# Kernel optimization log

Hardware: AMD Instinct MI355X
Metric: run time of the kernel (lower is better)

Reference implementation:

```python
import jax, jax.numpy as jnp
import numpy as np

E, C, FE, FS, K = 8, 1024, 1024, 4096, 2  # n_experts, embed, expert_inter, shared_inter, top_k
B, T = 4, 2048

def setup_inputs() -> dict:
    key = jax.random.key(0)
    ks = jax.random.split(key, 8)
    def init(k, shape, fan_in):
        return jax.random.normal(k, shape, jnp.float32) / np.sqrt(fan_in).astype(np.float32)
    return dict(
        x=jax.random.normal(ks[0], (B, T, C), jnp.float32),
        gate_w=init(ks[1], (E, C), C),        # nn.Linear(C, E, bias=False).weight
        ew1=init(ks[2], (E, C, FE), C),       # per-expert ln1 weights (transposed)
        ew2=init(ks[3], (E, C, FE), C),       # per-expert ln2 weights
        ewp=init(ks[4], (E, FE, C), FE),      # per-expert proj weights
        sw1=init(ks[5], (C, FS), C),          # shared FFN ln1
        sw2=init(ks[6], (C, FS), C),          # shared FFN ln2
        swp=init(ks[7], (FS, C), FS),         # shared FFN proj
    )

def reference(x, gate_w, ew1, ew2, ewp, sw1, sw2, swp):
    Bd, Td, Cd = x.shape
    xf = x.reshape(-1, Cd)                               # [N, C]
    scores = xf @ gate_w.T                               # [N, E] (eval mode: no noise)
    probs = jax.nn.softmax(scores, axis=-1)
    weights, indices = jax.lax.top_k(probs, K)           # [N, K]
    N = xf.shape[0]
    # combine[n, e] = routing weight of expert e for token n (0 if not selected)
    combine = jnp.zeros((N, E), xf.dtype).at[jnp.arange(N)[:, None], indices].add(weights)
    y = jnp.zeros_like(xf)
    for i in range(E):  # fixed small expert count; masked-dense replaces torch gather/scatter
        h = jax.nn.silu(xf @ ew1[i]) * (xf @ ew2[i])     # [N, FE] SwiGLU
        y = y + (h @ ewp[i]) * combine[:, i:i + 1]
    z = (jax.nn.silu(xf @ sw1) * (xf @ sw2)) @ swp       # shared expert (dropout p=0)
    return (y + z).reshape(Bd, Td, Cd), scores
```

## Files before the change

kernel.cpp:

```cpp
#include <hip/hip_runtime.h>

typedef unsigned short u16;
typedef unsigned int u32;
typedef __bf16 bf16x8 __attribute__((ext_vector_type(8)));
typedef float f32x4 __attribute__((ext_vector_type(4)));
typedef u16 u16x8 __attribute__((ext_vector_type(8)));

#define NTOK 8192
#define CDIM 1024
#define NEXP 8
#define FEDIM 1024
#define FSDIM 4096

#define GLD16(gp, lp) __builtin_amdgcn_global_load_lds( \
    (const __attribute__((address_space(1))) void*)(gp), \
    (__attribute__((address_space(3))) void*)(lp), 16, 0, 0)

__device__ __forceinline__ u16 f2bf(float f) {
  u32 u = __float_as_uint(f);
  u += 0x7FFFu + ((u >> 16) & 1u);
  return (u16)(u >> 16);
}

__global__ __launch_bounds__(256) void gate_kernel(
    const float* __restrict__ x, const float* __restrict__ gw,
    float* __restrict__ scores, u16* __restrict__ xb, int* __restrict__ cnt,
    int* __restrict__ tok, float* __restrict__ wgt)
{
  __shared__ int lcnt[NEXP];
  __shared__ int lbase[NEXP];
  __shared__ int rec_i[32];
  __shared__ int rec_p1[32], rec_p2[32];
  __shared__ float rec_w1[32], rec_w2[32];

  int tid = threadIdx.x, wave = tid >> 6, lane = tid & 63;
  if (tid < NEXP) lcnt[tid] = 0;
  __syncthreads();

  int tbase = blockIdx.x * 32 + wave * 8;
#pragma unroll
  for (int it = 0; it < 8; ++it) {
    int n = tbase + it;
    const float4* xr = (const float4*)(x + (size_t)n * CDIM) + lane * 4;
    float4 xv[4];
#pragma unroll
    for (int j = 0; j < 4; j++) xv[j] = xr[j];
    u16x8 rA, rB;
    rA[0]=f2bf(xv[0].x); rA[1]=f2bf(xv[0].y); rA[2]=f2bf(xv[0].z); rA[3]=f2bf(xv[0].w);
    rA[4]=f2bf(xv[1].x); rA[5]=f2bf(xv[1].y); rA[6]=f2bf(xv[1].z); rA[7]=f2bf(xv[1].w);
    rB[0]=f2bf(xv[2].x); rB[1]=f2bf(xv[2].y); rB[2]=f2bf(xv[2].z); rB[3]=f2bf(xv[2].w);
    rB[4]=f2bf(xv[3].x); rB[5]=f2bf(xv[3].y); rB[6]=f2bf(xv[3].z); rB[7]=f2bf(xv[3].w);
    u16* xrow = xb + (size_t)n * CDIM + lane * 16;
    *(u16x8*)xrow = rA;
    *(u16x8*)(xrow + 8) = rB;

    float s[NEXP];
#pragma unroll
    for (int e = 0; e < NEXP; e++) {
      const float4* g = (const float4*)(gw + (size_t)e * CDIM) + lane * 4;
      float a = 0.f;
#pragma unroll
      for (int j = 0; j < 4; j++) {
        float4 gv = g[j];
        a += xv[j].x * gv.x + xv[j].y * gv.y + xv[j].z * gv.z + xv[j].w * gv.w;
      }
#pragma unroll
      for (int o = 32; o > 0; o >>= 1) a += __shfl_xor(a, o);
      s[e] = a;
    }
    if (lane == 0) {
      float m = s[0];
      for (int e = 1; e < NEXP; e++) m = fmaxf(m, s[e]);
      float p[NEXP], sum = 0.f;
      for (int e = 0; e < NEXP; e++) { p[e] = __expf(s[e] - m); sum += p[e]; }
      int i1 = 0;
      for (int e = 1; e < NEXP; e++) if (p[e] > p[i1]) i1 = e;
      int i2 = (i1 == 0) ? 1 : 0;
      for (int e = 0; e < NEXP; e++) if (e != i1 && p[e] > p[i2]) i2 = e;
      float w1 = p[i1] / sum, w2 = p[i2] / sum;
#pragma unroll
      for (int e = 0; e < NEXP; e++) scores[(size_t)n * NEXP + e] = s[e];
      int p1 = atomicAdd(&lcnt[i1], 1);
      int p2 = atomicAdd(&lcnt[i2], 1);
      int slot = wave * 8 + it;
      rec_i[slot] = i1 | (i2 << 8);
      rec_p1[slot] = p1; rec_p2[slot] = p2;
      rec_w1[slot] = w1; rec_w2[slot] = w2;
    }
  }
  __syncthreads();
  if (tid < NEXP) lbase[tid] = atomicAdd(&cnt[tid], lcnt[tid]);
  __syncthreads();
  if (tid < 32) {
    int n = blockIdx.x * 32 + tid;
    int i1 = rec_i[tid] & 0xff, i2 = rec_i[tid] >> 8;
    int q1 = lbase[i1] + rec_p1[tid];
    int q2 = lbase[i2] + rec_p2[tid];
    tok[i1 * NTOK + q1] = n; wgt[i1 * NTOK + q1] = rec_w1[tid];
    tok[i2 * NTOK + q2] = n; wgt[i2 * NTOK + q2] = rec_w2[tid];
  }
}

__global__ void prefix_kernel(const int* __restrict__ cnt, int* __restrict__ prefix) {
  if (threadIdx.x == 0 && blockIdx.x == 0) {
    int a = 0;
    for (int e = 0; e < NEXP; e++) { prefix[e] = a; a += cnt[e]; }
    prefix[NEXP] = a;
  }
}

__global__ __launch_bounds__(256) void transpose_kernel(const float* __restrict__ src,
    u16* __restrict__ dst, int R, int C)
{
  __shared__ float tile[32][33];
  size_t base = (size_t)blockIdx.z * R * C;
  int c0 = blockIdx.x * 32, r0 = blockIdx.y * 32;
  int tx = threadIdx.x & 31, ty = threadIdx.x >> 5;
#pragma unroll
  for (int i = 0; i < 4; i++) {
    int r = ty + i * 8;
    tile[r][tx] = src[base + (size_t)(r0 + r) * C + c0 + tx];
  }
  __syncthreads();
#pragma unroll
  for (int i = 0; i < 4; i++) {
    int c = ty + i * 8;
    dst[base + (size_t)(c0 + c) * R + r0 + tx] = f2bf(tile[tx][c]);
  }
}

__global__ __launch_bounds__(256) void transpose_i_kernel(
    const float* __restrict__ s1, const float* __restrict__ s2,
    u16* __restrict__ dst, int R, int C, size_t sstride, size_t dstride)
{
  __shared__ float t1[32][33], t2[32][33];
  size_t sbase = (size_t)blockIdx.z * sstride;
  size_t dbase = (size_t)blockIdx.z * dstride;
  int c0 = blockIdx.x * 32, r0 = blockIdx.y * 32;
  int tx = threadIdx.x & 31, ty = threadIdx.x >> 5;
#pragma unroll
  for (int i = 0; i < 4; i++) {
    int r = ty + i * 8;
    t1[r][tx] = s1[sbase + (size_t)(r0 + r) * C + c0 + tx];
    t2[r][tx] = s2[sbase + (size_t)(r0 + r) * C + c0 + tx];
  }
  __syncthreads();
#pragma unroll
  for (int i = 0; i < 4; i++) {
    int c = ty + i * 8;
    dst[dbase + (size_t)(2 * (c0 + c) + 0) * R + r0 + tx] = f2bf(t1[tx][c]);
    dst[dbase + (size_t)(2 * (c0 + c) + 1) * R + r0 + tx] = f2bf(t2[tx][c]);
  }
}

#define BM2 256
#define BK2 64

template<int EPI, int AMODE, int BN_>
__global__ __launch_bounds__(512, 2) void gemm256(
    const u16* __restrict__ A, int lda,
    const u16* __restrict__ B, size_t bstride, int ldb,
    int M, int K,
    u16* __restrict__ Hout, int ldh,
    float* __restrict__ outF, int ldo,
    const int* __restrict__ cnt, const int* __restrict__ prefix,
    const int* __restrict__ tok, const float* __restrict__ wgt)
{
  constexpr int WN = BN_ / 4;
  constexpr int N_REP = WN / 16;
  constexpr int ACH = 4;
  constexpr int BCH = BN_ / 64;

  int e = blockIdx.z;
  int Mloc = (AMODE == 0) ? M : cnt[e];
  int mbase = blockIdx.y * BM2;
  if (AMODE != 0 && mbase >= Mloc) return;
  int nbase = blockIdx.x * BN_;
  int tid = threadIdx.x;
  int lane = tid & 63;
  int wid = tid >> 6;
  int wr = wid >> 2, wc = wid & 3;
  int fr = lane & 15;

  __shared__ __align__(16) u16 As[2][BM2 * BK2];
  __shared__ __align__(16) u16 Bs[2][BN_ * BK2];

  int srow = tid >> 3;
  int scol = ((tid & 7) ^ (srow & 7)) * 8;
  int pfx = (AMODE == 0) ? 0 : prefix[e];

  size_t arow[ACH];
#pragma unroll
  for (int c = 0; c < ACH; c++) {
    int rloc = mbase + c * 64 + srow;
    if (AMODE == 0)      arow[c] = rloc;
    else if (AMODE == 1) arow[c] = tok[e * NTOK + min(rloc, Mloc - 1)];
    else                 arow[c] = pfx + min(rloc, Mloc - 1);
  }
  const u16* Aps[ACH];
#pragma unroll
  for (int c = 0; c < ACH; c++) Aps[c] = A + arow[c] * (size_t)lda + scol;
  const u16* Bb = B + ((AMODE != 0) ? (size_t)e * bstride : 0);
  const u16* Bps[BCH];
#pragma unroll
  for (int c = 0; c < BCH; c++)
    Bps[c] = Bb + (size_t)(nbase + c * 64 + srow) * ldb + scol;

  auto STAGE = [&](int buf, int kof) {
#pragma unroll
    for (int c = 0; c < ACH; c++) GLD16(Aps[c] + kof, &As[buf][c * 4096 + tid * 8]);
#pragma unroll
    for (int c = 0; c < BCH; c++) GLD16(Bps[c] + kof, &Bs[buf][c * 4096 + tid * 8]);
  };

  f32x4 acc[8][N_REP] = {};

  auto COMPUTE = [&](int buf) {
#pragma unroll
    for (int ks = 0; ks < 2; ks++) {
      int slot = ((((ks << 2) + (lane >> 4)) ^ (fr & 7)) << 3);
      const u16* as = &As[buf][(wr * 128 + fr) * BK2 + slot];
      const u16* bs = &Bs[buf][(wc * WN + fr) * BK2 + slot];
      bf16x8 bfr[N_REP];
#pragma unroll
      for (int n = 0; n < N_REP; n++)
        bfr[n] = *(const bf16x8*)&bs[n * 1024];
#pragma unroll
      for (int m = 0; m < 8; m++) {
        bf16x8 af = *(const bf16x8*)&as[m * 1024];
#pragma unroll
        for (int n = 0; n < N_REP; n++)
          acc[m][n] = __builtin_amdgcn_mfma_f32_16x16x32_bf16(af, bfr[n], acc[m][n], 0, 0, 0);
      }
    }
  };

  int nt = K / BK2;
  STAGE(0, 0);
  STAGE(1, BK2);
  if constexpr (ACH + BCH == 8) asm volatile("s_waitcnt vmcnt(8)" ::: "memory");
  else                          asm volatile("s_waitcnt vmcnt(6)" ::: "memory");
  __builtin_amdgcn_s_barrier();
  __builtin_amdgcn_sched_barrier(0);

  for (int t = 0; t < nt; ++t) {
    COMPUTE(t & 1);
    __builtin_amdgcn_sched_barrier(0);
    if (t + 2 < nt) {
      __builtin_amdgcn_s_barrier();
      STAGE(t & 1, (t + 2) * BK2);
      if constexpr (ACH + BCH == 8) asm volatile("s_waitcnt vmcnt(8)" ::: "memory");
      else                          asm volatile("s_waitcnt vmcnt(6)" ::: "memory");
      __builtin_amdgcn_s_barrier();
      __builtin_amdgcn_sched_barrier(0);
    } else if (t + 1 < nt) {
      __builtin_amdgcn_s_barrier();
      asm volatile("s_waitcnt vmcnt(0)" ::: "memory");
      __builtin_amdgcn_s_barrier();
      __builtin_amdgcn_sched_barrier(0);
    }
  }

#pragma unroll
  for (int m = 0; m < 8; m++) {
#pragma unroll
    for (int j = 0; j < 4; j++) {
      int rloc = wr * 128 + m * 16 + (lane >> 4) * 4 + j;
      int rr = mbase + rloc;
      if (AMODE != 0 && rr >= Mloc) continue;
      int tk = 0; float wv = 0.f;
      if (EPI == 4) { tk = tok[e * NTOK + rr]; wv = wgt[e * NTOK + rr]; }
#pragma unroll
      for (int n = 0; n < N_REP; n++) {
        int wcol = wc * WN + n * 16 + fr;
        float v = acc[m][n][j];
        if (EPI == 0) {
          float o = __shfl_xor(v, 1);
          float g  = (fr & 1) ? o : v;
          float vv = (fr & 1) ? v : o;
          float hv = (g / (1.f + __expf(-g))) * vv;
          if (!(fr & 1))
            Hout[(size_t)(pfx + rr) * ldh + ((nbase + wcol) >> 1)] = f2bf(hv);
        } else if (EPI == 2) {
          outF[(size_t)rr * ldo + nbase + wcol] = v;
        } else {
          unsafeAtomicAdd(&outF[(size_t)tk * ldo + nbase + wcol], v * wv);
        }
      }
    }
  }
}

extern "C" void kernel_launch(void* const* d_in, const int* in_sizes, int n_in,
                              void* d_out, int out_size, void* d_ws, size_t ws_size,
                              hipStream_t stream)
{
  const float* x   = (const float*)d_in[0];
  const float* gw  = (const float*)d_in[1];
  const float* ew1 = (const float*)d_in[2];
  const float* ew2 = (const float*)d_in[3];
  const float* ewp = (const float*)d_in[4];
  const float* sw1 = (const float*)d_in[5];
  const float* sw2 = (const float*)d_in[6];
  const float* swp = (const float*)d_in[7];
  float* out    = (float*)d_out;
  float* scores = out + (size_t)NTOK * CDIM;

  char* wsp = (char*)d_ws;
  size_t off = 0;
  auto alloc = [&](size_t bytes) -> void* {
    void* p = wsp + off; off += (bytes + 255) & ~(size_t)255; return p;
  };
  u16* xb   = (u16*)alloc((size_t)NTOK * CDIM * 2);
  u16* swi  = (u16*)alloc((size_t)2 * FSDIM * CDIM * 2);
  u16* ewi  = (u16*)alloc((size_t)NEXP * 2 * FEDIM * CDIM * 2);
  u16* swpt = (u16*)alloc((size_t)CDIM * FSDIM * 2);
  u16* ewpt = (u16*)alloc((size_t)NEXP * CDIM * FEDIM * 2);
  u16* hs   = (u16*)alloc((size_t)NTOK * FSDIM * 2);
  u16* he   = (u16*)alloc((size_t)2 * NTOK * FEDIM * 2);
  int* cnt  = (int*)alloc(256);
  int* pfx  = (int*)alloc(256);
  int* tok  = (int*)alloc((size_t)NEXP * NTOK * 4);
  float* wgt = (float*)alloc((size_t)NEXP * NTOK * 4);
  if (off > ws_size) return;

  hipMemsetAsync(cnt, 0, 32, stream);
  gate_kernel<<<NTOK / 32, 256, 0, stream>>>(x, gw, scores, xb, cnt, tok, wgt);
  prefix_kernel<<<1, 64, 0, stream>>>(cnt, pfx);
  transpose_i_kernel<<<dim3(FSDIM/32, CDIM/32, 1), 256, 0, stream>>>(
      sw1, sw2, swi, CDIM, FSDIM, 0, 0);
  transpose_i_kernel<<<dim3(FEDIM/32, CDIM/32, NEXP), 256, 0, stream>>>(
      ew1, ew2, ewi, CDIM, FEDIM, (size_t)CDIM * FEDIM, (size_t)2 * FEDIM * CDIM);
  transpose_kernel<<<dim3(CDIM/32, FSDIM/32, 1), 256, 0, stream>>>(swp, swpt, FSDIM, CDIM);
  transpose_kernel<<<dim3(CDIM/32, FEDIM/32, NEXP), 256, 0, stream>>>(ewp, ewpt, FEDIM, CDIM);

  gemm256<0,0,256><<<dim3(2*FSDIM/256, NTOK/256, 1), 512, 0, stream>>>(
      xb, CDIM, swi, 0, CDIM, NTOK, CDIM, hs, FSDIM, nullptr, 0,
      nullptr, nullptr, nullptr, nullptr);
  gemm256<2,0,128><<<dim3(CDIM/128, NTOK/256, 1), 512, 0, stream>>>(
      hs, FSDIM, swpt, 0, FSDIM, NTOK, FSDIM, nullptr, 0, out, CDIM,
      nullptr, nullptr, nullptr, nullptr);

  gemm256<0,1,256><<<dim3(2*FEDIM/256, NTOK/256, NEXP), 512, 0, stream>>>(
      xb, CDIM, ewi, (size_t)2 * FEDIM * CDIM, CDIM, 0, CDIM, he, FEDIM, nullptr, 0,
      cnt, pfx, tok, nullptr);
  gemm256<4,2,128><<<dim3(CDIM/128, NTOK/256, NEXP), 512, 0, stream>>>(
      he, FEDIM, ewpt, (size_t)CDIM * FEDIM, FEDIM, 0, FEDIM, nullptr, 0, out, CDIM,
      cnt, pfx, tok, wgt);
}
```

Measured before the change: 608.2 us.

## Restructure GEMM main loop into four-phase ping-pong schedule with priority hints

Replaces the two-tiles-ahead prefetch loop with a one-tile-ahead double buffer. Each K-step is split into four phases that interleave LDS fragment reads and MFMA quarters, with workgroup barriers and s_setprio raising wave priority around the MFMA blocks. The intent is to let waves alternate between memory and matrix work, hiding LDS and global load latency better. The cost is many more barriers per iteration and a shallower global prefetch, which could expose global load latency.

```diff
diff --git a/kernel.cpp b/kernel.cpp
--- a/kernel.cpp
+++ b/kernel.cpp
@@ -215,50 +215,90 @@
 
   f32x4 acc[8][N_REP] = {};
 
-  auto COMPUTE = [&](int buf) {
-#pragma unroll
-    for (int ks = 0; ks < 2; ks++) {
-      int slot = ((((ks << 2) + (lane >> 4)) ^ (fr & 7)) << 3);
-      const u16* as = &As[buf][(wr * 128 + fr) * BK2 + slot];
-      const u16* bs = &Bs[buf][(wc * WN + fr) * BK2 + slot];
-      bf16x8 bfr[N_REP];
-#pragma unroll
-      for (int n = 0; n < N_REP; n++)
-        bfr[n] = *(const bf16x8*)&bs[n * 1024];
-#pragma unroll
-      for (int m = 0; m < 8; m++) {
-        bf16x8 af = *(const bf16x8*)&as[m * 1024];
-#pragma unroll
-        for (int n = 0; n < N_REP; n++)
-          acc[m][n] = __builtin_amdgcn_mfma_f32_16x16x32_bf16(af, bfr[n], acc[m][n], 0, 0, 0);
-      }
-    }
-  };
-
   int nt = K / BK2;
   STAGE(0, 0);
-  STAGE(1, BK2);
-  if constexpr (ACH + BCH == 8) asm volatile("s_waitcnt vmcnt(8)" ::: "memory");
-  else                          asm volatile("s_waitcnt vmcnt(6)" ::: "memory");
+  asm volatile("s_waitcnt vmcnt(0)" ::: "memory");
   __builtin_amdgcn_s_barrier();
   __builtin_amdgcn_sched_barrier(0);
 
+  int slot0 = (((lane >> 4)) ^ (fr & 7)) << 3;
+  int slot1 = ((4 + (lane >> 4)) ^ (fr & 7)) << 3;
+
   for (int t = 0; t < nt; ++t) {
-    COMPUTE(t & 1);
-    __builtin_amdgcn_sched_barrier(0);
-    if (t + 2 < nt) {
-      __builtin_amdgcn_s_barrier();
-      STAGE(t & 1, (t + 2) * BK2);
-      if constexpr (ACH + BCH == 8) asm volatile("s_waitcnt vmcnt(8)" ::: "memory");
-      else                          asm volatile("s_waitcnt vmcnt(6)" ::: "memory");
-      __builtin_amdgcn_s_barrier();
-      __builtin_amdgcn_sched_barrier(0);
-    } else if (t + 1 < nt) {
-      __builtin_amdgcn_s_barrier();
-      asm volatile("s_waitcnt vmcnt(0)" ::: "memory");
-      __builtin_amdgcn_s_barrier();
-      __builtin_amdgcn_sched_barrier(0);
-    }
+    int c = t & 1;
+    bool pf = (t + 1 < nt);
+    const u16* asb = &As[c][(wr * 128 + fr) * BK2];
+    const u16* bsb = &Bs[c][(wc * WN + fr) * BK2];
+
+    bf16x8 b0[N_REP], a0[4];
+#pragma unroll
+    for (int n = 0; n < N_REP; n++) b0[n] = *(const bf16x8*)&bsb[n * 1024 + slot0];
+#pragma unroll
+    for (int m = 0; m < 4; m++) a0[m] = *(const bf16x8*)&asb[m * 1024 + slot0];
+    if (pf) STAGE(c ^ 1, (t + 1) * BK2);
+    __builtin_amdgcn_s_barrier();
+    asm volatile("s_waitcnt lgkmcnt(0)" ::: "memory");
+    __builtin_amdgcn_sched_barrier(0);
+    __builtin_amdgcn_s_setprio(1);
+#pragma unroll
+    for (int m = 0; m < 4; m++)
+#pragma unroll
+      for (int n = 0; n < N_REP; n++)
+        acc[m][n] = __builtin_amdgcn_mfma_f32_16x16x32_bf16(a0[m], b0[n], acc[m][n], 0, 0, 0);
+    __builtin_amdgcn_s_setprio(0);
+    __builtin_amdgcn_s_barrier();
+    __builtin_amdgcn_sched_barrier(0);
+
+    bf16x8 a1[4];
+#pragma unroll
+    for (int m = 0; m < 4; m++) a1[m] = *(const bf16x8*)&asb[(4 + m) * 1024 + slot0];
+    __builtin_amdgcn_s_barrier();
+    asm volatile("s_waitcnt lgkmcnt(0)" ::: "memory");
+    __builtin_amdgcn_sched_barrier(0);
+    __builtin_amdgcn_s_setprio(1);
+#pragma unroll
+    for (int m = 0; m < 4; m++)
+#pragma unroll
+      for (int n = 0; n < N_REP; n++)
+        acc[4 + m][n] = __builtin_amdgcn_mfma_f32_16x16x32_bf16(a1[m], b0[n], acc[4 + m][n], 0, 0, 0);
+    __builtin_amdgcn_s_setprio(0);
+    __builtin_amdgcn_s_barrier();
+    __builtin_amdgcn_sched_barrier(0);
+
+    bf16x8 b1[N_REP], a2[4];
+#pragma unroll
+    for (int n = 0; n < N_REP; n++) b1[n] = *(const bf16x8*)&bsb[n * 1024 + slot1];
+#pragma unroll
+    for (int m = 0; m < 4; m++) a2[m] = *(const bf16x8*)&asb[(4 + m) * 1024 + slot1];
+    __builtin_amdgcn_s_barrier();
+    asm volatile("s_waitcnt lgkmcnt(0)" ::: "memory");
+    __builtin_amdgcn_sched_barrier(0);
+    __builtin_amdgcn_s_setprio(1);
+#pragma unroll
+    for (int m = 0; m < 4; m++)
+#pragma unroll
+      for (int n = 0; n < N_REP; n++)
+        acc[4 + m][n] = __builtin_amdgcn_mfma_f32_16x16x32_bf16(a2[m], b1[n], acc[4 + m][n], 0, 0, 0);
+    __builtin_amdgcn_s_setprio(0);
+    __builtin_amdgcn_s_barrier();
+    __builtin_amdgcn_sched_barrier(0);
+
+    bf16x8 a3[4];
+#pragma unroll
+    for (int m = 0; m < 4; m++) a3[m] = *(const bf16x8*)&asb[m * 1024 + slot1];
+    __builtin_amdgcn_s_barrier();
+    asm volatile("s_waitcnt lgkmcnt(0)" ::: "memory");
+    __builtin_amdgcn_sched_barrier(0);
+    __builtin_amdgcn_s_setprio(1);
+#pragma unroll
+    for (int m = 0; m < 4; m++)
+#pragma unroll
+      for (int n = 0; n < N_REP; n++)
+        acc[m][n] = __builtin_amdgcn_mfma_f32_16x16x32_bf16(a3[m], b1[n], acc[m][n], 0, 0, 0);
+    __builtin_amdgcn_s_setprio(0);
+    if (pf) asm volatile("s_waitcnt vmcnt(0)" ::: "memory");
+    __builtin_amdgcn_s_barrier();
+    __builtin_amdgcn_sched_barrier(0);
   }
 
 #pragma unroll
```

Result: no change. 615.3 us (+1.2%).
